# Performance work log

Hardware: AMD Instinct MI355X
Metric: run time of the kernel (lower is better)

The kernel has to match this reference:

```python
import jax, jax.numpy as jnp
import numpy as np

DIM = 1024
H = 16
HD = 64

def setup_inputs() -> dict:
    key = jax.random.key(0)
    ks = jax.random.split(key, 5)
    x = jax.random.normal(ks[0], (2, 2048, DIM), dtype=jnp.float32)
    gamma = jnp.ones((DIM,), jnp.float32)
    beta = jnp.zeros((DIM,), jnp.float32)
    w_qkv = jax.random.normal(ks[1], (DIM, 3 * H * HD), dtype=jnp.float32) * (DIM ** -0.5)
    w_out = jax.random.normal(ks[2], (H * HD, DIM), dtype=jnp.float32) * ((H * HD) ** -0.5)
    b_out = jnp.zeros((DIM,), jnp.float32)
    return {"x": x, "gamma": gamma, "beta": beta, "w_qkv": w_qkv, "w_out": w_out, "b_out": b_out}

def reference(x, gamma, beta, w_qkv, w_out, b_out):
    # LayerNorm (pre-norm)
    mu = jnp.mean(x, axis=-1, keepdims=True)
    var = jnp.var(x, axis=-1, keepdims=True)
    xn = (x - mu) * jax.lax.rsqrt(var + 1e-5) * gamma + beta
    # QKV projection (no bias)
    qkv = xn @ w_qkv  # (b, n, 3*h*hd)
    q, k, v = jnp.split(qkv, 3, axis=-1)
    b, n, _ = x.shape
    split = lambda t: t.reshape(b, n, H, HD).transpose(0, 2, 1, 3)  # b h n d
    q, k, v = split(q), split(k), split(v)
    scale = HD ** -0.5
    scores = jnp.einsum('bhqd,bhkd->bhqk', q, k) * scale
    weights = jax.nn.softmax(scores, axis=-1)
    attn = jnp.einsum('bhqk,bhkd->bhqd', weights, v)  # b h n d
    attn = attn.transpose(0, 2, 1, 3).reshape(b, n, H * HD)
    # output projection (dropout is identity in eval)
    return attn @ w_out + b_out
```

## Files before the change

### kernel.cpp

```cpp
#include <hip/hip_runtime.h>
#include <hip/hip_bf16.h>


typedef _Float16 f16x8 __attribute__((ext_vector_type(8)));
typedef _Float16 f16x4 __attribute__((ext_vector_type(4)));
typedef float    f32x4 __attribute__((ext_vector_type(4)));

#define DIM   1024
#define NH    16
#define HD2   64
#define SEQ   2048
#define ROWS  4096
#define QKVN  3072

__device__ __forceinline__ void async_copy16(void* lds, const void* gsrc) {
    __builtin_amdgcn_global_load_lds(
        (const __attribute__((address_space(1))) unsigned int*)gsrc,
        (__attribute__((address_space(3))) unsigned int*)lds, 16, 0, 0);
}

__global__ __launch_bounds__(256) void ln_kernel(
    const float* __restrict__ x, const float* __restrict__ gamma,
    const float* __restrict__ beta, _Float16* __restrict__ xn) {
    const int row = blockIdx.x;
    const int t = threadIdx.x;
    const float4 v = reinterpret_cast<const float4*>(x + (size_t)row * DIM)[t];
    float s1 = v.x + v.y + v.z + v.w;
    float s2 = v.x * v.x + v.y * v.y + v.z * v.z + v.w * v.w;
    for (int off = 32; off; off >>= 1) {
        s1 += __shfl_down(s1, off);
        s2 += __shfl_down(s2, off);
    }
    __shared__ float red[8];
    const int wv = t >> 6, lane = t & 63;
    if (lane == 0) { red[wv * 2] = s1; red[wv * 2 + 1] = s2; }
    __syncthreads();
    s1 = red[0] + red[2] + red[4] + red[6];
    s2 = red[1] + red[3] + red[5] + red[7];
    const float mu = s1 * (1.0f / DIM);
    const float var = s2 * (1.0f / DIM) - mu * mu;
    const float rstd = rsqrtf(var + 1e-5f);
    const float4 g = reinterpret_cast<const float4*>(gamma)[t];
    const float4 bb = reinterpret_cast<const float4*>(beta)[t];
    f16x4 o;
    o[0] = (_Float16)((v.x - mu) * rstd * g.x + bb.x);
    o[1] = (_Float16)((v.y - mu) * rstd * g.y + bb.y);
    o[2] = (_Float16)((v.z - mu) * rstd * g.z + bb.z);
    o[3] = (_Float16)((v.w - mu) * rstd * g.w + bb.w);
    reinterpret_cast<f16x4*>(xn + (size_t)row * DIM)[t] = o;
}

__global__ __launch_bounds__(256) void transpose_cvt_kernel(
    const float* __restrict__ in, _Float16* __restrict__ out, int R, int C) {
    __shared__ float tile[32][33];
    const int c0 = blockIdx.x * 32, r0 = blockIdx.y * 32;
    const int tx = threadIdx.x, ty = threadIdx.y;
#pragma unroll
    for (int i = 0; i < 4; i++)
        tile[ty + i * 8][tx] = in[(size_t)(r0 + ty + i * 8) * C + c0 + tx];
    __syncthreads();
#pragma unroll
    for (int i = 0; i < 4; i++)
        out[(size_t)(c0 + ty + i * 8) * R + r0 + tx] = (_Float16)tile[tx][ty + i * 8];
}

__global__ __launch_bounds__(256) void gemm_qkv_kernel(
    const _Float16* __restrict__ A, const _Float16* __restrict__ Bt,
    _Float16* __restrict__ qk, _Float16* __restrict__ vT, int K) {
    __shared__ _Float16 Al[128 * 32];
    __shared__ _Float16 Bl[128 * 32];
    const int t = threadIdx.x, wv = t >> 6, lane = t & 63;
    const int lg = lane >> 4, lr = lane & 15;
    const int wr = wv >> 1, wc = wv & 1;
    const int m0 = blockIdx.y * 128, n0 = blockIdx.x * 128;

    f32x4 acc[4][4] = {};

    const int srow = t >> 2, sk = (t & 3) * 8;
    const _Float16* Ag0 = A + (size_t)(m0 + srow) * K + sk;
    const _Float16* Bg0 = Bt + (size_t)(n0 + srow) * K + sk;
    _Float16* Alw = Al + wv * 512;
    _Float16* Blw = Bl + wv * 512;

    for (int k0 = 0; k0 < K; k0 += 32) {
        __syncthreads();
        async_copy16(Alw,        Ag0 + k0);
        async_copy16(Alw + 2048, Ag0 + (size_t)64 * K + k0);
        async_copy16(Blw,        Bg0 + k0);
        async_copy16(Blw + 2048, Bg0 + (size_t)64 * K + k0);
        __syncthreads();
        f16x8 af[4], bfr[4];
#pragma unroll
        for (int m = 0; m < 4; m++)
            af[m] = *reinterpret_cast<const f16x8*>(&Al[(wr * 64 + m * 16 + lr) * 32 + lg * 8]);
#pragma unroll
        for (int n = 0; n < 4; n++)
            bfr[n] = *reinterpret_cast<const f16x8*>(&Bl[(wc * 64 + n * 16 + lr) * 32 + lg * 8]);
#pragma unroll
        for (int m = 0; m < 4; m++)
#pragma unroll
            for (int n = 0; n < 4; n++)
                acc[m][n] = __builtin_amdgcn_mfma_f32_16x16x32_f16(af[m], bfr[n], acc[m][n], 0, 0, 0);
    }

    if (n0 < 2 * DIM) {
#pragma unroll
        for (int m = 0; m < 4; m++) {
            const int row = m0 + wr * 64 + m * 16 + lg * 4;
#pragma unroll
            for (int n = 0; n < 4; n++) {
                const int col = n0 + wc * 64 + n * 16 + lr;
#pragma unroll
                for (int jj = 0; jj < 4; jj++)
                    qk[(size_t)(row + jj) * 2048 + col] = (_Float16)acc[m][n][jj];
            }
        }
    } else {
#pragma unroll
        for (int m = 0; m < 4; m++) {
            const int row = m0 + wr * 64 + m * 16 + lg * 4;
            const int b = row >> 11, nn = row & 2047;
#pragma unroll
            for (int n = 0; n < 4; n++) {
                const int vcol = n0 + wc * 64 + n * 16 + lr - 2 * DIM;
                f16x4 pk;
#pragma unroll
                for (int jj = 0; jj < 4; jj++) pk[jj] = (_Float16)acc[m][n][jj];
                *reinterpret_cast<f16x4*>(&vT[(size_t)(b * 1024 + vcol) * SEQ + nn]) = pk;
            }
        }
    }
}

__global__ __launch_bounds__(256) void gemm_out_kernel(
    const _Float16* __restrict__ A, const _Float16* __restrict__ Bt,
    float* __restrict__ C, const float* __restrict__ bias, int N, int K) {
    __shared__ _Float16 Al[128 * 32];
    __shared__ _Float16 Bl[128 * 32];
    const int t = threadIdx.x, wv = t >> 6, lane = t & 63;
    const int lg = lane >> 4, lr = lane & 15;
    const int wr = wv >> 1, wc = wv & 1;
    const int m0 = blockIdx.y * 128, n0 = blockIdx.x * 128;

    f32x4 acc[4][4] = {};

    const int srow = t >> 2, sk = (t & 3) * 8;
    const _Float16* Ag0 = A + (size_t)(m0 + srow) * K + sk;
    const _Float16* Bg0 = Bt + (size_t)(n0 + srow) * K + sk;
    _Float16* Alw = Al + wv * 512;
    _Float16* Blw = Bl + wv * 512;

    for (int k0 = 0; k0 < K; k0 += 32) {
        __syncthreads();
        async_copy16(Alw,        Ag0 + k0);
        async_copy16(Alw + 2048, Ag0 + (size_t)64 * K + k0);
        async_copy16(Blw,        Bg0 + k0);
        async_copy16(Blw + 2048, Bg0 + (size_t)64 * K + k0);
        __syncthreads();
        f16x8 af[4], bfr[4];
#pragma unroll
        for (int m = 0; m < 4; m++)
            af[m] = *reinterpret_cast<const f16x8*>(&Al[(wr * 64 + m * 16 + lr) * 32 + lg * 8]);
#pragma unroll
        for (int n = 0; n < 4; n++)
            bfr[n] = *reinterpret_cast<const f16x8*>(&Bl[(wc * 64 + n * 16 + lr) * 32 + lg * 8]);
#pragma unroll
        for (int m = 0; m < 4; m++)
#pragma unroll
            for (int n = 0; n < 4; n++)
                acc[m][n] = __builtin_amdgcn_mfma_f32_16x16x32_f16(af[m], bfr[n], acc[m][n], 0, 0, 0);
    }

#pragma unroll
    for (int m = 0; m < 4; m++) {
        const int row = m0 + wr * 64 + m * 16 + lg * 4;
#pragma unroll
        for (int n = 0; n < 4; n++) {
            const int col = n0 + wc * 64 + n * 16 + lr;
            const float bo = bias[col];
#pragma unroll
            for (int jj = 0; jj < 4; jj++)
                C[(size_t)(row + jj) * N + col] = acc[m][n][jj] + bo;
        }
    }
}

__global__ __launch_bounds__(256) void attn_fa_kernel(
    const _Float16* __restrict__ qk, const _Float16* __restrict__ vT,
    _Float16* __restrict__ attn) {
    const int bh = blockIdx.y, b = bh >> 4, h = bh & 15;
    const int q0 = blockIdx.x * 64;
    const int t = threadIdx.x, wv = t >> 6, lane = t & 63;
    const int lg = lane >> 4, lr = lane & 15;

    __shared__ _Float16 Kl[64][72];
    __shared__ _Float16 Vt[64][72];
    __shared__ _Float16 PT[4][16][72];

    const size_t qrow = (size_t)(b * SEQ + q0 + wv * 16 + lr);
    const _Float16* qp = qk + qrow * 2048 + h * HD2;
    f16x8 qf0 = *reinterpret_cast<const f16x8*>(qp + lg * 8);
    f16x8 qf1 = *reinterpret_cast<const f16x8*>(qp + 32 + lg * 8);
    qf0 = qf0 * (_Float16)0.125f;
    qf1 = qf1 * (_Float16)0.125f;

    f32x4 o[4] = {};
    float mrun = -INFINITY, lrun = 0.f;

    const int sr = t >> 3, sc = (t & 7) * 8;
    const _Float16* kbase = qk + (size_t)(b * SEQ + sr) * 2048 + DIM + h * HD2 + sc;
    const _Float16* vbase = vT + (size_t)(bh * HD2 + sr) * SEQ + sc;

    for (int kv0 = 0; kv0 < SEQ; kv0 += 64) {
        __syncthreads();
        {
            const _Float16* kp = kbase + (size_t)kv0 * 2048;
            *reinterpret_cast<f16x8*>(&Kl[sr][sc])      = *reinterpret_cast<const f16x8*>(kp);
            *reinterpret_cast<f16x8*>(&Kl[sr + 32][sc]) = *reinterpret_cast<const f16x8*>(kp + (size_t)32 * 2048);
            const _Float16* vp = vbase + kv0;
            *reinterpret_cast<f16x8*>(&Vt[sr][sc])      = *reinterpret_cast<const f16x8*>(vp);
            *reinterpret_cast<f16x8*>(&Vt[sr + 32][sc]) = *reinterpret_cast<const f16x8*>(vp + (size_t)32 * SEQ);
        }
        __syncthreads();

        f32x4 s[4];
#pragma unroll
        for (int n = 0; n < 4; n++) {
            f16x8 kf0 = *reinterpret_cast<const f16x8*>(&Kl[n * 16 + lr][lg * 8]);
            f16x8 kf1 = *reinterpret_cast<const f16x8*>(&Kl[n * 16 + lr][32 + lg * 8]);
            f32x4 z = {0.f, 0.f, 0.f, 0.f};
            z = __builtin_amdgcn_mfma_f32_16x16x32_f16(kf0, qf0, z, 0, 0, 0);
            z = __builtin_amdgcn_mfma_f32_16x16x32_f16(kf1, qf1, z, 0, 0, 0);
            s[n] = z;
        }

        float m1 = -INFINITY;
#pragma unroll
        for (int n = 0; n < 4; n++)
            m1 = fmaxf(m1, fmaxf(fmaxf(s[n][0], s[n][1]), fmaxf(s[n][2], s[n][3])));
        m1 = fmaxf(m1, __shfl_xor(m1, 16));
        m1 = fmaxf(m1, __shfl_xor(m1, 32));
        const float mnew = fmaxf(mrun, m1);
        const float corr = __expf(mrun - mnew);
        mrun = mnew;
        float rsum = 0.f;
#pragma unroll
        for (int n = 0; n < 4; n++)
#pragma unroll
            for (int jj = 0; jj < 4; jj++) {
                const float p = __expf(s[n][jj] - mnew);
                s[n][jj] = p;
                rsum += p;
            }
        rsum += __shfl_xor(rsum, 16);
        rsum += __shfl_xor(rsum, 32);
        lrun = lrun * corr + rsum;
#pragma unroll
        for (int dn = 0; dn < 4; dn++) o[dn] *= corr;

#pragma unroll
        for (int n = 0; n < 4; n++) {
            f16x4 pk;
#pragma unroll
            for (int jj = 0; jj < 4; jj++) pk[jj] = (_Float16)s[n][jj];
            *reinterpret_cast<f16x4*>(&PT[wv][lr][n * 16 + lg * 4]) = pk;
        }
        f16x8 pa0 = *reinterpret_cast<const f16x8*>(&PT[wv][lr][lg * 8]);
        f16x8 pa1 = *reinterpret_cast<const f16x8*>(&PT[wv][lr][32 + lg * 8]);

#pragma unroll
        for (int dn = 0; dn < 4; dn++) {
            f16x8 vf0 = *reinterpret_cast<const f16x8*>(&Vt[dn * 16 + lr][lg * 8]);
            f16x8 vf1 = *reinterpret_cast<const f16x8*>(&Vt[dn * 16 + lr][32 + lg * 8]);
            o[dn] = __builtin_amdgcn_mfma_f32_16x16x32_f16(vf0, pa0, o[dn], 0, 0, 0);
            o[dn] = __builtin_amdgcn_mfma_f32_16x16x32_f16(vf1, pa1, o[dn], 0, 0, 0);
        }
    }

    const float inv = 1.0f / lrun;
    const size_t orow = (size_t)(b * SEQ + q0 + wv * 16 + lr);
#pragma unroll
    for (int dn = 0; dn < 4; dn++) {
        f16x4 pk;
#pragma unroll
        for (int jj = 0; jj < 4; jj++) pk[jj] = (_Float16)(o[dn][jj] * inv);
        *reinterpret_cast<f16x4*>(&attn[orow * DIM + h * HD2 + dn * 16 + lg * 4]) = pk;
    }
}

extern "C" void kernel_launch(void* const* d_in, const int* in_sizes, int n_in,
                              void* d_out, int out_size, void* d_ws, size_t ws_size,
                              hipStream_t stream) {
    const float* x     = (const float*)d_in[0];
    const float* gamma = (const float*)d_in[1];
    const float* beta  = (const float*)d_in[2];
    const float* w_qkv = (const float*)d_in[3];
    const float* w_out = (const float*)d_in[4];
    const float* b_out = (const float*)d_in[5];
    float* out = (float*)d_out;

    _Float16* ws    = (_Float16*)d_ws;
    _Float16* xn    = ws;
    _Float16* wqkvT = xn + (size_t)ROWS * DIM;
    _Float16* woutT = wqkvT + (size_t)QKVN * DIM;
    _Float16* qk    = woutT + (size_t)DIM * DIM;
    _Float16* vT    = qk + (size_t)ROWS * 2048;
    _Float16* attnb = xn;

    ln_kernel<<<ROWS, 256, 0, stream>>>(x, gamma, beta, xn);
    transpose_cvt_kernel<<<dim3(QKVN / 32, DIM / 32), dim3(32, 8), 0, stream>>>(w_qkv, wqkvT, DIM, QKVN);
    transpose_cvt_kernel<<<dim3(DIM / 32, DIM / 32), dim3(32, 8), 0, stream>>>(w_out, woutT, DIM, DIM);
    gemm_qkv_kernel<<<dim3(QKVN / 128, ROWS / 128), 256, 0, stream>>>(xn, wqkvT, qk, vT, DIM);
    attn_fa_kernel<<<dim3(SEQ / 64, 32), 256, 0, stream>>>(qk, vT, attnb);
    gemm_out_kernel<<<dim3(DIM / 128, ROWS / 128), 256, 0, stream>>>(attnb, woutT, out, b_out, DIM, DIM);
}
```

Measured before the change: 230.2 us.

## Double-buffer GEMMs, prefetch KV in registers, lazy softmax rescale, remap attention blocks

Both GEMMs now double-buffer their LDS tiles so the next k-slice loads while the current one runs on MFMA. The output GEMM tile is narrowed to 64 columns to launch more blocks. Attention prefetches the next K/V tile into registers, remaps block ids to group heads per XCD, and raises wave priority around MFMAs. It also skips the running-max rescale unless the max grows by more than 8. These aim to hide memory latency and cut exp/rescale work, at the cost of more LDS and registers and looser bounds on the fp16 probabilities.

```diff
diff --git a/kernel.cpp b/kernel.cpp
--- a/kernel.cpp
+++ b/kernel.cpp
@@ -67,8 +67,8 @@
 __global__ __launch_bounds__(256) void gemm_qkv_kernel(
     const _Float16* __restrict__ A, const _Float16* __restrict__ Bt,
     _Float16* __restrict__ qk, _Float16* __restrict__ vT, int K) {
-    __shared__ _Float16 Al[128 * 32];
-    __shared__ _Float16 Bl[128 * 32];
+    __shared__ _Float16 Al[2][128 * 32];
+    __shared__ _Float16 Bl[2][128 * 32];
     const int t = threadIdx.x, wv = t >> 6, lane = t & 63;
     const int lg = lane >> 4, lr = lane & 15;
     const int wr = wv >> 1, wc = wv & 1;
@@ -79,28 +79,39 @@
     const int srow = t >> 2, sk = (t & 3) * 8;
     const _Float16* Ag0 = A + (size_t)(m0 + srow) * K + sk;
     const _Float16* Bg0 = Bt + (size_t)(n0 + srow) * K + sk;
-    _Float16* Alw = Al + wv * 512;
-    _Float16* Blw = Bl + wv * 512;
-
-    for (int k0 = 0; k0 < K; k0 += 32) {
-        __syncthreads();
+
+    auto STAGE = [&](int buf, int k0) {
+        _Float16* Alw = &Al[buf][wv * 512];
+        _Float16* Blw = &Bl[buf][wv * 512];
         async_copy16(Alw,        Ag0 + k0);
         async_copy16(Alw + 2048, Ag0 + (size_t)64 * K + k0);
         async_copy16(Blw,        Bg0 + k0);
         async_copy16(Blw + 2048, Bg0 + (size_t)64 * K + k0);
-        __syncthreads();
+    };
+
+    STAGE(0, 0);
+    asm volatile("s_waitcnt vmcnt(0)" ::: "memory");
+    __builtin_amdgcn_s_barrier();
+    int cur = 0;
+    for (int k0 = 0; k0 < K; k0 += 32) {
+        if (k0 + 32 < K) STAGE(cur ^ 1, k0 + 32);
+        const _Float16* Ab = &Al[cur][0];
+        const _Float16* Bb = &Bl[cur][0];
         f16x8 af[4], bfr[4];
 #pragma unroll
         for (int m = 0; m < 4; m++)
-            af[m] = *reinterpret_cast<const f16x8*>(&Al[(wr * 64 + m * 16 + lr) * 32 + lg * 8]);
+            af[m] = *reinterpret_cast<const f16x8*>(&Ab[(wr * 64 + m * 16 + lr) * 32 + lg * 8]);
 #pragma unroll
         for (int n = 0; n < 4; n++)
-            bfr[n] = *reinterpret_cast<const f16x8*>(&Bl[(wc * 64 + n * 16 + lr) * 32 + lg * 8]);
+            bfr[n] = *reinterpret_cast<const f16x8*>(&Bb[(wc * 64 + n * 16 + lr) * 32 + lg * 8]);
 #pragma unroll
         for (int m = 0; m < 4; m++)
 #pragma unroll
             for (int n = 0; n < 4; n++)
                 acc[m][n] = __builtin_amdgcn_mfma_f32_16x16x32_f16(af[m], bfr[n], acc[m][n], 0, 0, 0);
+        asm volatile("s_waitcnt vmcnt(0)" ::: "memory");
+        __builtin_amdgcn_s_barrier();
+        cur ^= 1;
     }
 
     if (n0 < 2 * DIM) {
@@ -135,48 +146,58 @@
 __global__ __launch_bounds__(256) void gemm_out_kernel(
     const _Float16* __restrict__ A, const _Float16* __restrict__ Bt,
     float* __restrict__ C, const float* __restrict__ bias, int N, int K) {
-    __shared__ _Float16 Al[128 * 32];
-    __shared__ _Float16 Bl[128 * 32];
+    __shared__ _Float16 Al[2][128 * 32];
+    __shared__ _Float16 Bl[2][64 * 32];
     const int t = threadIdx.x, wv = t >> 6, lane = t & 63;
     const int lg = lane >> 4, lr = lane & 15;
     const int wr = wv >> 1, wc = wv & 1;
-    const int m0 = blockIdx.y * 128, n0 = blockIdx.x * 128;
-
-    f32x4 acc[4][4] = {};
+    const int m0 = blockIdx.y * 128, n0 = blockIdx.x * 64;
+
+    f32x4 acc[4][2] = {};
 
     const int srow = t >> 2, sk = (t & 3) * 8;
     const _Float16* Ag0 = A + (size_t)(m0 + srow) * K + sk;
     const _Float16* Bg0 = Bt + (size_t)(n0 + srow) * K + sk;
-    _Float16* Alw = Al + wv * 512;
-    _Float16* Blw = Bl + wv * 512;
-
-    for (int k0 = 0; k0 < K; k0 += 32) {
-        __syncthreads();
+
+    auto STAGE = [&](int buf, int k0) {
+        _Float16* Alw = &Al[buf][wv * 512];
+        _Float16* Blw = &Bl[buf][wv * 512];
         async_copy16(Alw,        Ag0 + k0);
         async_copy16(Alw + 2048, Ag0 + (size_t)64 * K + k0);
         async_copy16(Blw,        Bg0 + k0);
-        async_copy16(Blw + 2048, Bg0 + (size_t)64 * K + k0);
-        __syncthreads();
-        f16x8 af[4], bfr[4];
+    };
+
+    STAGE(0, 0);
+    asm volatile("s_waitcnt vmcnt(0)" ::: "memory");
+    __builtin_amdgcn_s_barrier();
+    int cur = 0;
+    for (int k0 = 0; k0 < K; k0 += 32) {
+        if (k0 + 32 < K) STAGE(cur ^ 1, k0 + 32);
+        const _Float16* Ab = &Al[cur][0];
+        const _Float16* Bb = &Bl[cur][0];
+        f16x8 af[4], bfr[2];
 #pragma unroll
         for (int m = 0; m < 4; m++)
-            af[m] = *reinterpret_cast<const f16x8*>(&Al[(wr * 64 + m * 16 + lr) * 32 + lg * 8]);
-#pragma unroll
-        for (int n = 0; n < 4; n++)
-            bfr[n] = *reinterpret_cast<const f16x8*>(&Bl[(wc * 64 + n * 16 + lr) * 32 + lg * 8]);
+            af[m] = *reinterpret_cast<const f16x8*>(&Ab[(wr * 64 + m * 16 + lr) * 32 + lg * 8]);
+#pragma unroll
+        for (int n = 0; n < 2; n++)
+            bfr[n] = *reinterpret_cast<const f16x8*>(&Bb[(wc * 32 + n * 16 + lr) * 32 + lg * 8]);
 #pragma unroll
         for (int m = 0; m < 4; m++)
 #pragma unroll
-            for (int n = 0; n < 4; n++)
+            for (int n = 0; n < 2; n++)
                 acc[m][n] = __builtin_amdgcn_mfma_f32_16x16x32_f16(af[m], bfr[n], acc[m][n], 0, 0, 0);
+        asm volatile("s_waitcnt vmcnt(0)" ::: "memory");
+        __builtin_amdgcn_s_barrier();
+        cur ^= 1;
     }
 
 #pragma unroll
     for (int m = 0; m < 4; m++) {
         const int row = m0 + wr * 64 + m * 16 + lg * 4;
 #pragma unroll
-        for (int n = 0; n < 4; n++) {
-            const int col = n0 + wc * 64 + n * 16 + lr;
+        for (int n = 0; n < 2; n++) {
+            const int col = n0 + wc * 32 + n * 16 + lr;
             const float bo = bias[col];
 #pragma unroll
             for (int jj = 0; jj < 4; jj++)
@@ -188,8 +209,10 @@
 __global__ __launch_bounds__(256) void attn_fa_kernel(
     const _Float16* __restrict__ qk, const _Float16* __restrict__ vT,
     _Float16* __restrict__ attn) {
-    const int bh = blockIdx.y, b = bh >> 4, h = bh & 15;
-    const int q0 = blockIdx.x * 64;
+    const int id = blockIdx.x;
+    const int nid = (id & 7) * 128 + (id >> 3);
+    const int bh = nid >> 5, b = bh >> 4, h = bh & 15;
+    const int q0 = (nid & 31) * 64;
     const int t = threadIdx.x, wv = t >> 6, lane = t & 63;
     const int lg = lane >> 4, lr = lane & 15;
 
@@ -211,17 +234,27 @@
     const _Float16* kbase = qk + (size_t)(b * SEQ + sr) * 2048 + DIM + h * HD2 + sc;
     const _Float16* vbase = vT + (size_t)(bh * HD2 + sr) * SEQ + sc;
 
+    f16x8 rk0 = *reinterpret_cast<const f16x8*>(kbase);
+    f16x8 rk1 = *reinterpret_cast<const f16x8*>(kbase + (size_t)32 * 2048);
+    f16x8 rv0 = *reinterpret_cast<const f16x8*>(vbase);
+    f16x8 rv1 = *reinterpret_cast<const f16x8*>(vbase + (size_t)32 * SEQ);
+
     for (int kv0 = 0; kv0 < SEQ; kv0 += 64) {
-        __syncthreads();
-        {
-            const _Float16* kp = kbase + (size_t)kv0 * 2048;
-            *reinterpret_cast<f16x8*>(&Kl[sr][sc])      = *reinterpret_cast<const f16x8*>(kp);
-            *reinterpret_cast<f16x8*>(&Kl[sr + 32][sc]) = *reinterpret_cast<const f16x8*>(kp + (size_t)32 * 2048);
-            const _Float16* vp = vbase + kv0;
-            *reinterpret_cast<f16x8*>(&Vt[sr][sc])      = *reinterpret_cast<const f16x8*>(vp);
-            *reinterpret_cast<f16x8*>(&Vt[sr + 32][sc]) = *reinterpret_cast<const f16x8*>(vp + (size_t)32 * SEQ);
-        }
-        __syncthreads();
+        __builtin_amdgcn_s_barrier();
+        *reinterpret_cast<f16x8*>(&Kl[sr][sc])      = rk0;
+        *reinterpret_cast<f16x8*>(&Kl[sr + 32][sc]) = rk1;
+        *reinterpret_cast<f16x8*>(&Vt[sr][sc])      = rv0;
+        *reinterpret_cast<f16x8*>(&Vt[sr + 32][sc]) = rv1;
+        if (kv0 + 64 < SEQ) {
+            const _Float16* kp = kbase + (size_t)(kv0 + 64) * 2048;
+            const _Float16* vp = vbase + (kv0 + 64);
+            rk0 = *reinterpret_cast<const f16x8*>(kp);
+            rk1 = *reinterpret_cast<const f16x8*>(kp + (size_t)32 * 2048);
+            rv0 = *reinterpret_cast<const f16x8*>(vp);
+            rv1 = *reinterpret_cast<const f16x8*>(vp + (size_t)32 * SEQ);
+        }
+        asm volatile("s_waitcnt lgkmcnt(0)" ::: "memory");
+        __builtin_amdgcn_s_barrier();
 
         f32x4 s[4];
 #pragma unroll
@@ -229,34 +262,39 @@
             f16x8 kf0 = *reinterpret_cast<const f16x8*>(&Kl[n * 16 + lr][lg * 8]);
             f16x8 kf1 = *reinterpret_cast<const f16x8*>(&Kl[n * 16 + lr][32 + lg * 8]);
             f32x4 z = {0.f, 0.f, 0.f, 0.f};
+            __builtin_amdgcn_s_setprio(1);
             z = __builtin_amdgcn_mfma_f32_16x16x32_f16(kf0, qf0, z, 0, 0, 0);
             z = __builtin_amdgcn_mfma_f32_16x16x32_f16(kf1, qf1, z, 0, 0, 0);
+            __builtin_amdgcn_s_setprio(0);
             s[n] = z;
         }
 
-        float m1 = -INFINITY;
-#pragma unroll
-        for (int n = 0; n < 4; n++)
+        float m1 = fmaxf(fmaxf(s[0][0], s[0][1]), fmaxf(s[0][2], s[0][3]));
+#pragma unroll
+        for (int n = 1; n < 4; n++)
             m1 = fmaxf(m1, fmaxf(fmaxf(s[n][0], s[n][1]), fmaxf(s[n][2], s[n][3])));
         m1 = fmaxf(m1, __shfl_xor(m1, 16));
         m1 = fmaxf(m1, __shfl_xor(m1, 32));
-        const float mnew = fmaxf(mrun, m1);
-        const float corr = __expf(mrun - mnew);
-        mrun = mnew;
+        if (!__all(m1 - mrun <= 8.f)) {
+            const float mnew = fmaxf(mrun, m1);
+            const float corr = __expf(mrun - mnew);
+            mrun = mnew;
+            lrun *= corr;
+#pragma unroll
+            for (int dn = 0; dn < 4; dn++) o[dn] *= corr;
+        }
         float rsum = 0.f;
 #pragma unroll
         for (int n = 0; n < 4; n++)
 #pragma unroll
             for (int jj = 0; jj < 4; jj++) {
-                const float p = __expf(s[n][jj] - mnew);
+                const float p = __expf(s[n][jj] - mrun);
                 s[n][jj] = p;
                 rsum += p;
             }
         rsum += __shfl_xor(rsum, 16);
         rsum += __shfl_xor(rsum, 32);
-        lrun = lrun * corr + rsum;
-#pragma unroll
-        for (int dn = 0; dn < 4; dn++) o[dn] *= corr;
+        lrun += rsum;
 
 #pragma unroll
         for (int n = 0; n < 4; n++) {
@@ -272,8 +310,10 @@
         for (int dn = 0; dn < 4; dn++) {
             f16x8 vf0 = *reinterpret_cast<const f16x8*>(&Vt[dn * 16 + lr][lg * 8]);
             f16x8 vf1 = *reinterpret_cast<const f16x8*>(&Vt[dn * 16 + lr][32 + lg * 8]);
+            __builtin_amdgcn_s_setprio(1);
             o[dn] = __builtin_amdgcn_mfma_f32_16x16x32_f16(vf0, pa0, o[dn], 0, 0, 0);
             o[dn] = __builtin_amdgcn_mfma_f32_16x16x32_f16(vf1, pa1, o[dn], 0, 0, 0);
+            __builtin_amdgcn_s_setprio(0);
         }
     }
 
@@ -311,6 +351,6 @@
     transpose_cvt_kernel<<<dim3(QKVN / 32, DIM / 32), dim3(32, 8), 0, stream>>>(w_qkv, wqkvT, DIM, QKVN);
     transpose_cvt_kernel<<<dim3(DIM / 32, DIM / 32), dim3(32, 8), 0, stream>>>(w_out, woutT, DIM, DIM);
     gemm_qkv_kernel<<<dim3(QKVN / 128, ROWS / 128), 256, 0, stream>>>(xn, wqkvT, qk, vT, DIM);
-    attn_fa_kernel<<<dim3(SEQ / 64, 32), 256, 0, stream>>>(qk, vT, attnb);
-    gemm_out_kernel<<<dim3(DIM / 128, ROWS / 128), 256, 0, stream>>>(attnb, woutT, out, b_out, DIM, DIM);
-}
+    attn_fa_kernel<<<1024, 256, 0, stream>>>(qk, vT, attnb);
+    gemm_out_kernel<<<dim3(DIM / 64, ROWS / 128), 256, 0, stream>>>(attnb, woutT, out, b_out, DIM, DIM);
+}
```

Result: faster. 217.2 us (-5.6%).
